# Optimization experiments

Hardware: AMD Instinct MI355X
Metric: run time of the kernel (lower is better)

Reference implementation:

```python
import jax, jax.numpy as jnp
import numpy as np

B, S, D, H = 2, 2048, 1024, 16
HD = D // H  # head_dim = 64


def setup_inputs() -> dict:
    key = jax.random.key(0)
    ks = jax.random.split(key, 6)
    scale = 0.02
    x = jax.random.normal(ks[0], (B, S, D), dtype=jnp.float32)
    Wq = jax.random.normal(ks[1], (D, D), dtype=jnp.float32) * scale
    Wk = jax.random.normal(ks[2], (D, D), dtype=jnp.float32) * scale
    Wv = jax.random.normal(ks[3], (D, D), dtype=jnp.float32) * scale
    Wo = jax.random.normal(ks[4], (D, D), dtype=jnp.float32) * scale
    bo = jnp.zeros((D,), dtype=jnp.float32)
    return {"x": x, "Wq": Wq, "Wk": Wk, "Wv": Wv, "Wo": Wo, "bo": bo}


def reference(x, Wq, Wk, Wv, Wo, bo):
    b, s, _ = x.shape
    # Linear projections (qkv_bias=False), split into heads: [b, h, s, hd]
    def split_heads(t):
        return t.reshape(b, s, H, HD).transpose(0, 2, 1, 3)
    q = split_heads(x @ Wq)
    k = split_heads(x @ Wk)
    v = split_heads(x @ Wv)
    # Scaled dot-product scores: [b, h, s, s]
    scores = jnp.einsum('bhqd,bhkd->bhqk', q, k) / jnp.sqrt(jnp.float32(HD))
    # Causal mask: triu(ones, diagonal=1) positions -> -inf
    causal = jnp.triu(jnp.ones((s, s), dtype=bool), k=1)
    scores = jnp.where(causal, -jnp.inf, scores)
    attn = jax.nn.softmax(scores, axis=-1)
    # dropout p=0.0 (eval-equivalent): identity
    ctx = jnp.einsum('bhqk,bhkd->bhqd', attn, v)  # [b, h, s, hd]
    ctx = ctx.transpose(0, 2, 1, 3).reshape(b, s, D)
    return ctx @ Wo + bo
```

## Files before the change

### kernel.cpp

```cpp
#include <hip/hip_runtime.h>
#include <math.h>

#define BB 2
#define SS 2048
#define DD 1024
#define HH 16
#define HD 64
#define MM (BB * SS)

typedef __bf16 bf16;
typedef __attribute__((ext_vector_type(8))) __bf16 bf16x8;
typedef __attribute__((ext_vector_type(4))) __bf16 bf16x4;
typedef __attribute__((ext_vector_type(4))) float f32x4;

__device__ __forceinline__ void gld_lds16(const void* g, void* l) {
    __builtin_amdgcn_global_load_lds(
        (const __attribute__((address_space(1))) void*)g,
        (__attribute__((address_space(3))) void*)l, 16, 0, 0);
}

__global__ __launch_bounds__(256) void prep(
    const float* __restrict__ x,
    const float* __restrict__ W0, const float* __restrict__ W1,
    const float* __restrict__ W2, const float* __restrict__ W3,
    bf16* __restrict__ xb, bf16* __restrict__ Wt)
{
    __shared__ float tile[32][33];
    const int z = blockIdx.z;
    if (z < 4) {
        const float* W = (z == 0) ? W0 : (z == 1) ? W1 : (z == 2) ? W2 : W3;
        bf16* O = Wt + (size_t)z * DD * DD;
        const int tx = threadIdx.x & 31, ty = threadIdx.x >> 5;
        const int k0 = blockIdx.y * 32, n0 = blockIdx.x * 32;
#pragma unroll
        for (int i = 0; i < 4; ++i)
            tile[ty + i * 8][tx] = W[(size_t)(k0 + ty + i * 8) * DD + n0 + tx];
        __syncthreads();
#pragma unroll
        for (int i = 0; i < 4; ++i)
            O[(size_t)(n0 + ty + i * 8) * DD + k0 + tx] = (bf16)tile[tx][ty + i * 8];
    } else {
        const int lb = (z - 4) * 1024 + blockIdx.y * 32 + blockIdx.x;
        const size_t i = ((size_t)lb * 256 + threadIdx.x) * 8;
        const float4 a = *(const float4*)(x + i);
        const float4 b = *(const float4*)(x + i + 4);
        bf16x8 o;
        o[0] = (bf16)a.x; o[1] = (bf16)a.y; o[2] = (bf16)a.z; o[3] = (bf16)a.w;
        o[4] = (bf16)b.x; o[5] = (bf16)b.y; o[6] = (bf16)b.z; o[7] = (bf16)b.w;
        *(bf16x8*)(xb + i) = o;
    }
}

template<bool SWAP>
__device__ __forceinline__ void mfma_core(
    const bf16* __restrict__ A, const bf16* __restrict__ Bt,
    int bm, int bn, int K, bf16* As, bf16* Bs, f32x4 (&acc)[4][4])
{
    const int t = threadIdx.x;
    const int w = t >> 6;
    const int l16 = t & 15, quad = (t >> 4) & 3;
    const int wr = w >> 1, wc = w & 1;
    const int r0 = t >> 3;
    const int cs = t & 7;

    for (int k0 = 0; k0 < K; k0 += 64) {
#pragma unroll
        for (int j = 0; j < 4; ++j) {
            const int row = j * 32 + r0;
            const int c = (cs - row) & 7;
            gld_lds16(A  + (size_t)(bm + row) * K + k0 + c * 8,
                      As + (j * 32 + w * 8) * 64);
            gld_lds16(Bt + (size_t)(bn + row) * K + k0 + c * 8,
                      Bs + (j * 32 + w * 8) * 64);
        }
        __syncthreads();

#pragma unroll
        for (int h = 0; h < 2; ++h) {
            bf16x8 af[4], bv[4];
#pragma unroll
            for (int i = 0; i < 4; ++i) {
                const int ra = wr * 64 + i * 16 + l16;
                af[i] = *(const bf16x8*)(As + ra * 64 + (((h * 4 + quad) + ra) & 7) * 8);
                const int rb = wc * 64 + i * 16 + l16;
                bv[i] = *(const bf16x8*)(Bs + rb * 64 + (((h * 4 + quad) + rb) & 7) * 8);
            }
#pragma unroll
            for (int mi = 0; mi < 4; ++mi)
#pragma unroll
                for (int ni = 0; ni < 4; ++ni)
                    acc[mi][ni] = SWAP
                        ? __builtin_amdgcn_mfma_f32_16x16x32_bf16(bv[mi], af[ni], acc[mi][ni], 0, 0, 0)
                        : __builtin_amdgcn_mfma_f32_16x16x32_bf16(af[mi], bv[ni], acc[mi][ni], 0, 0, 0);
        }
        __syncthreads();
    }
}

__global__ __launch_bounds__(256) void gemm_qkv(
    const bf16* __restrict__ xb, const bf16* __restrict__ Wt,
    bf16* __restrict__ Qb, bf16* __restrict__ Kb, bf16* __restrict__ Vb)
{
    __shared__ __align__(16) bf16 As[128 * 64];
    __shared__ __align__(16) bf16 Bs[128 * 64];
    const int bm = blockIdx.y * 128, bn = blockIdx.x * 128, z = blockIdx.z;
    const bf16* Wz = Wt + (size_t)z * DD * DD;

    const int t = threadIdx.x;
    const int w = t >> 6, l16 = t & 15, quad = (t >> 4) & 3;
    const int wr = w >> 1, wc = w & 1;

    f32x4 acc[4][4] = {};
    if (z < 2) {
        mfma_core<true>(xb, Wz, bm, bn, DD, As, Bs, acc);
        bf16* outp = (z == 0) ? Qb : Kb;
#pragma unroll
        for (int mi = 0; mi < 4; ++mi) {
            const int feat = bn + wc * 64 + mi * 16 + quad * 4;
            const int h = feat >> 6, hd = feat & 63;
#pragma unroll
            for (int ni = 0; ni < 4; ++ni) {
                const int tok = bm + wr * 64 + ni * 16 + l16;
                const int b = tok >> 11, s = tok & (SS - 1);
                bf16x4 o;
#pragma unroll
                for (int r = 0; r < 4; ++r) o[r] = (bf16)acc[mi][ni][r];
                *(bf16x4*)(outp + ((size_t)((b * HH + h) * SS + s)) * HD + hd) = o;
            }
        }
    } else {
        mfma_core<false>(xb, Wz, bm, bn, DD, As, Bs, acc);
#pragma unroll
        for (int mi = 0; mi < 4; ++mi) {
            const int tok0 = bm + wr * 64 + mi * 16 + quad * 4;
            const int b = tok0 >> 11, s0 = tok0 & (SS - 1);
#pragma unroll
            for (int ni = 0; ni < 4; ++ni) {
                const int feat = bn + wc * 64 + ni * 16 + l16;
                const int h = feat >> 6, hd = feat & 63;
                bf16x4 o;
#pragma unroll
                for (int r = 0; r < 4; ++r) o[r] = (bf16)acc[mi][ni][r];
                *(bf16x4*)(Vb + ((size_t)((b * HH + h) * HD + hd)) * SS + s0) = o;
            }
        }
    }
}

__global__ __launch_bounds__(256) void gemm_out(
    const bf16* __restrict__ ctx, const bf16* __restrict__ Wto,
    const float* __restrict__ bias, float* __restrict__ out)
{
    __shared__ __align__(16) bf16 As[128 * 64];
    __shared__ __align__(16) bf16 Bs[128 * 64];
    const int bm = blockIdx.y * 128, bn = blockIdx.x * 128;

    f32x4 acc[4][4] = {};
    mfma_core<true>(ctx, Wto, bm, bn, DD, As, Bs, acc);

    const int t = threadIdx.x;
    const int w = t >> 6, l16 = t & 15, quad = (t >> 4) & 3;
    const int wr = w >> 1, wc = w & 1;

#pragma unroll
    for (int mi = 0; mi < 4; ++mi) {
        const int feat = bn + wc * 64 + mi * 16 + quad * 4;
        const float4 bb = *(const float4*)(bias + feat);
#pragma unroll
        for (int ni = 0; ni < 4; ++ni) {
            const int tok = bm + wr * 64 + ni * 16 + l16;
            float4 o;
            o.x = acc[mi][ni][0] + bb.x;
            o.y = acc[mi][ni][1] + bb.y;
            o.z = acc[mi][ni][2] + bb.z;
            o.w = acc[mi][ni][3] + bb.w;
            *(float4*)(out + (size_t)tok * DD + feat) = o;
        }
    }
}

#define PROWS 72
__global__ __launch_bounds__(256) void attn_part(
    const bf16* __restrict__ Q, const bf16* __restrict__ K,
    const bf16* __restrict__ Vt, bf16* __restrict__ Op, float* __restrict__ Lp)
{
    __shared__ __align__(16) bf16 Ks[2][64 * 64];
    __shared__ __align__(16) bf16 Vs[2][64 * 64];
    __shared__ __align__(16) bf16 Pl[4][16 * PROWS];

    const int t = threadIdx.x;
    const int w = t >> 6;
    const int lane = t & 63;
    const int l16 = lane & 15, quad = lane >> 4;

    const int L    = blockIdx.x;
    const int bh   = L & 31;
    const int rest = L >> 5;
    const int part = rest & 1;
    const int qg   = 31 - (rest >> 1);
    const int n    = qg + 1;
    const int half = (n + 1) >> 1;
    const int kt_lo = part ? half : 0;
    const int kt_hi = part ? n : half;
    const int q0w  = qg * 64 + w * 16;

    const bf16* Qp = Q  + ((size_t)bh * SS + q0w) * HD;
    const bf16* Kp = K  + (size_t)bh * SS * HD;
    const bf16* Vp = Vt + (size_t)bh * HD * SS;
    bf16* Pw = &Pl[w][0];

    const bf16x8 bQ0 = *(const bf16x8*)(Qp + l16 * HD + quad * 8);
    const bf16x8 bQ1 = *(const bf16x8*)(Qp + l16 * HD + 32 + quad * 8);

    f32x4 accO[4] = {{0,0,0,0},{0,0,0,0},{0,0,0,0},{0,0,0,0}};
    float Lr = 0.f;
    const float cl2 = 0.125f * 1.44269504f;
    const int qrow = q0w + l16;

    const int r8 = lane >> 3, cs = lane & 7;

    if (kt_lo < kt_hi) {
        const int kb0 = kt_lo * 64;
#pragma unroll
        for (int j = 0; j < 2; ++j) {
            const int region = w * 2 + j;
            const int row = region * 8 + r8;
            const int c = (cs - row) & 7;
            gld_lds16(Kp + (size_t)(kb0 + row) * HD + c * 8, &Ks[0][region * 512]);
            gld_lds16(Vp + (size_t)row * SS + kb0 + c * 8, &Vs[0][region * 512]);
        }

        for (int kt = kt_lo; kt < kt_hi; ++kt) {
            const int kb = kt * 64;
            const int buf = (kt - kt_lo) & 1;
            __syncthreads();

            if (kt + 1 < kt_hi) {
                const int kb2 = kb + 64;
#pragma unroll
                for (int j = 0; j < 2; ++j) {
                    const int region = w * 2 + j;
                    const int row = region * 8 + r8;
                    const int c = (cs - row) & 7;
                    gld_lds16(Kp + (size_t)(kb2 + row) * HD + c * 8, &Ks[buf ^ 1][region * 512]);
                    gld_lds16(Vp + (size_t)row * SS + kb2 + c * 8, &Vs[buf ^ 1][region * 512]);
                }
            }

            const bf16* Kbuf = &Ks[buf][0];
            const bf16* Vbuf = &Vs[buf][0];

            f32x4 St[4] = {{0,0,0,0},{0,0,0,0},{0,0,0,0},{0,0,0,0}};
#pragma unroll
            for (int mi = 0; mi < 4; ++mi) {
                const int row = mi * 16 + l16;
                const bf16x8 a0 = *(const bf16x8*)(Kbuf + row * 64 + ((quad + row) & 7) * 8);
                const bf16x8 a1 = *(const bf16x8*)(Kbuf + row * 64 + ((quad + 4 + row) & 7) * 8);
                St[mi] = __builtin_amdgcn_mfma_f32_16x16x32_bf16(a0, bQ0, St[mi], 0, 0, 0);
                St[mi] = __builtin_amdgcn_mfma_f32_16x16x32_bf16(a1, bQ1, St[mi], 0, 0, 0);
            }

            if (kb + 63 > q0w) {
#pragma unroll
                for (int mi = 0; mi < 4; ++mi)
#pragma unroll
                    for (int r = 0; r < 4; ++r)
                        if (kb + mi * 16 + quad * 4 + r > qrow) St[mi][r] = -1e30f;
            }

            float rs = 0.f;
#pragma unroll
            for (int mi = 0; mi < 4; ++mi) {
                bf16x4 pk;
#pragma unroll
                for (int r = 0; r < 4; ++r) {
                    const float p = exp2f(St[mi][r] * cl2);
                    rs += p;
                    pk[r] = (bf16)p;
                }
                *(bf16x4*)(Pw + l16 * PROWS + mi * 16 + quad * 4) = pk;
            }
            rs += __shfl_xor(rs, 16);
            rs += __shfl_xor(rs, 32);
            Lr += rs;

#pragma unroll
            for (int kc = 0; kc < 2; ++kc) {
                const bf16x8 bP = *(const bf16x8*)(Pw + l16 * PROWS + kc * 32 + quad * 8);
#pragma unroll
                for (int mi = 0; mi < 4; ++mi) {
                    const int row = mi * 16 + l16;
                    const bf16x8 aV = *(const bf16x8*)(
                        Vbuf + row * 64 + (((kc * 4 + quad) + row) & 7) * 8);
                    accO[mi] = __builtin_amdgcn_mfma_f32_16x16x32_bf16(aV, bP, accO[mi], 0, 0, 0);
                }
            }
        }
    }

    bf16* op = Op + ((size_t)(part * 32 + bh) * SS + q0w + l16) * HD;
#pragma unroll
    for (int mi = 0; mi < 4; ++mi) {
        bf16x4 o;
#pragma unroll
        for (int r = 0; r < 4; ++r) o[r] = (bf16)accO[mi][r];
        *(bf16x4*)(op + mi * 16 + quad * 4) = o;
    }
    if (quad == 0)
        Lp[(size_t)(part * 32 + bh) * SS + q0w + l16] = Lr;
}

__global__ __launch_bounds__(256) void attn_combine(
    const bf16* __restrict__ Op, const float* __restrict__ Lp,
    bf16* __restrict__ ctx)
{
    const size_t i = ((size_t)blockIdx.x * 256 + threadIdx.x) * 8;
    const int d  = (int)(i & 63);
    const int q  = (int)((i >> 6) & (SS - 1));
    const int bh = (int)(i >> 17);

    const bf16x8 a = *(const bf16x8*)(Op + i);
    const bf16x8 b = *(const bf16x8*)(Op + (size_t)32 * SS * HD + i);
    const size_t lidx = i >> 6;
    const float rinv = 1.0f / (Lp[lidx] + Lp[(size_t)32 * SS + lidx]);

    bf16x8 o;
#pragma unroll
    for (int j = 0; j < 8; ++j)
        o[j] = (bf16)(((float)a[j] + (float)b[j]) * rinv);

    *(bf16x8*)(ctx + ((size_t)((bh >> 4) * SS + q)) * DD + (bh & 15) * 64 + d) = o;
}

extern "C" void kernel_launch(void* const* d_in, const int* in_sizes, int n_in,
                              void* d_out, int out_size, void* d_ws, size_t ws_size,
                              hipStream_t stream)
{
    const float* x  = (const float*)d_in[0];
    const float* Wq = (const float*)d_in[1];
    const float* Wk = (const float*)d_in[2];
    const float* Wv = (const float*)d_in[3];
    const float* Wo = (const float*)d_in[4];
    const float* bo = (const float*)d_in[5];
    float* out = (float*)d_out;

    const size_t chunk = (size_t)MM * DD;
    bf16* xb  = (bf16*)d_ws;
    bf16* Wt  = xb + chunk;
    bf16* Qb  = Wt + 4 * (size_t)DD * DD;
    bf16* Kb  = Qb + chunk;
    bf16* Vb  = Kb + chunk;
    bf16* ctx = Vb + chunk;
    bf16* Op  = ctx + chunk;
    float* Lp = (float*)(Op + 2 * (size_t)32 * SS * HD);

    prep<<<dim3(32, 32, 6), dim3(256), 0, stream>>>(x, Wq, Wk, Wv, Wo, xb, Wt);

    gemm_qkv<<<dim3(DD / 128, MM / 128, 3), dim3(256), 0, stream>>>(xb, Wt, Qb, Kb, Vb);

    attn_part<<<dim3(2048), dim3(256), 0, stream>>>(Qb, Kb, Vb, Op, Lp);
    attn_combine<<<dim3(2048), dim3(256), 0, stream>>>(Op, Lp, ctx);

    gemm_out<<<dim3(DD / 128, MM / 128), dim3(256), 0, stream>>>(
        ctx, Wt + 3 * (size_t)DD * DD, bo, out);
}
```

Baseline: 198.2 us.

## Replace split-K attention and combine with single-pass 128-row attention; retile output GEMM

Attention now gives each block 128 query rows (32 per wave) and walks the full causal key range in one pass. This removes the two-part key split, the partial-output buffers and the separate combine kernel, and normalises directly into ctx. Each K/V tile is reused across twice as many queries, at the cost of fewer blocks (512) and longer, more imbalanced per-block work. The output GEMM switches to 128x64 tiles over a 512-block 1D grid with its own inline load loop. That loop is single-buffered, so it has two syncs per k-step and no prefetch overlap.

```diff
diff --git a/kernel.cpp b/kernel.cpp
--- a/kernel.cpp
+++ b/kernel.cpp
@@ -152,184 +152,221 @@
     const float* __restrict__ bias, float* __restrict__ out)
 {
     __shared__ __align__(16) bf16 As[128 * 64];
-    __shared__ __align__(16) bf16 Bs[128 * 64];
-    const int bm = blockIdx.y * 128, bn = blockIdx.x * 128;
-
-    f32x4 acc[4][4] = {};
-    mfma_core<true>(ctx, Wto, bm, bn, DD, As, Bs, acc);
+    __shared__ __align__(16) bf16 Bs[64 * 64];
+
+    const int L = blockIdx.x;
+    const int bm = (L >> 4) * 128;
+    const int bn = (L & 15) * 64;
 
     const int t = threadIdx.x;
     const int w = t >> 6, l16 = t & 15, quad = (t >> 4) & 3;
     const int wr = w >> 1, wc = w & 1;
-
-#pragma unroll
-    for (int mi = 0; mi < 4; ++mi) {
-        const int feat = bn + wc * 64 + mi * 16 + quad * 4;
+    const int r0 = t >> 3, cs = t & 7;
+
+    f32x4 acc[2][4] = {};
+
+    for (int k0 = 0; k0 < DD; k0 += 64) {
+#pragma unroll
+        for (int j = 0; j < 4; ++j) {
+            const int row = j * 32 + r0;
+            const int c = (cs - row) & 7;
+            gld_lds16(ctx + (size_t)(bm + row) * DD + k0 + c * 8,
+                      As + (j * 32 + w * 8) * 64);
+        }
+#pragma unroll
+        for (int j = 0; j < 2; ++j) {
+            const int row = j * 32 + r0;
+            const int c = (cs - row) & 7;
+            gld_lds16(Wto + (size_t)(bn + row) * DD + k0 + c * 8,
+                      Bs + (j * 32 + w * 8) * 64);
+        }
+        __syncthreads();
+
+#pragma unroll
+        for (int h = 0; h < 2; ++h) {
+            bf16x8 af[4], bv[2];
+#pragma unroll
+            for (int i = 0; i < 4; ++i) {
+                const int ra = wr * 64 + i * 16 + l16;
+                af[i] = *(const bf16x8*)(As + ra * 64 + (((h * 4 + quad) + ra) & 7) * 8);
+            }
+#pragma unroll
+            for (int i = 0; i < 2; ++i) {
+                const int rb = wc * 32 + i * 16 + l16;
+                bv[i] = *(const bf16x8*)(Bs + rb * 64 + (((h * 4 + quad) + rb) & 7) * 8);
+            }
+#pragma unroll
+            for (int fi = 0; fi < 2; ++fi)
+#pragma unroll
+                for (int ti = 0; ti < 4; ++ti)
+                    acc[fi][ti] = __builtin_amdgcn_mfma_f32_16x16x32_bf16(
+                        bv[fi], af[ti], acc[fi][ti], 0, 0, 0);
+        }
+        __syncthreads();
+    }
+
+#pragma unroll
+    for (int fi = 0; fi < 2; ++fi) {
+        const int feat = bn + wc * 32 + fi * 16 + quad * 4;
         const float4 bb = *(const float4*)(bias + feat);
 #pragma unroll
-        for (int ni = 0; ni < 4; ++ni) {
-            const int tok = bm + wr * 64 + ni * 16 + l16;
+        for (int ti = 0; ti < 4; ++ti) {
+            const int tok = bm + wr * 64 + ti * 16 + l16;
             float4 o;
-            o.x = acc[mi][ni][0] + bb.x;
-            o.y = acc[mi][ni][1] + bb.y;
-            o.z = acc[mi][ni][2] + bb.z;
-            o.w = acc[mi][ni][3] + bb.w;
+            o.x = acc[fi][ti][0] + bb.x;
+            o.y = acc[fi][ti][1] + bb.y;
+            o.z = acc[fi][ti][2] + bb.z;
+            o.w = acc[fi][ti][3] + bb.w;
             *(float4*)(out + (size_t)tok * DD + feat) = o;
         }
     }
 }
 
 #define PROWS 72
-__global__ __launch_bounds__(256) void attn_part(
+__global__ __launch_bounds__(256) void attn_flash(
     const bf16* __restrict__ Q, const bf16* __restrict__ K,
-    const bf16* __restrict__ Vt, bf16* __restrict__ Op, float* __restrict__ Lp)
+    const bf16* __restrict__ Vt, bf16* __restrict__ ctx)
 {
     __shared__ __align__(16) bf16 Ks[2][64 * 64];
     __shared__ __align__(16) bf16 Vs[2][64 * 64];
-    __shared__ __align__(16) bf16 Pl[4][16 * PROWS];
+    __shared__ __align__(16) bf16 Pl[4][32 * PROWS];
 
     const int t = threadIdx.x;
     const int w = t >> 6;
     const int lane = t & 63;
     const int l16 = lane & 15, quad = lane >> 4;
 
-    const int L    = blockIdx.x;
-    const int bh   = L & 31;
-    const int rest = L >> 5;
-    const int part = rest & 1;
-    const int qg   = 31 - (rest >> 1);
-    const int n    = qg + 1;
-    const int half = (n + 1) >> 1;
-    const int kt_lo = part ? half : 0;
-    const int kt_hi = part ? n : half;
-    const int q0w  = qg * 64 + w * 16;
+    const int L  = blockIdx.x;
+    const int bh = L & 31;
+    const int qg = 15 - (L >> 5);
+    const int q0w = qg * 128 + w * 32;
 
     const bf16* Qp = Q  + ((size_t)bh * SS + q0w) * HD;
     const bf16* Kp = K  + (size_t)bh * SS * HD;
     const bf16* Vp = Vt + (size_t)bh * HD * SS;
     bf16* Pw = &Pl[w][0];
 
-    const bf16x8 bQ0 = *(const bf16x8*)(Qp + l16 * HD + quad * 8);
-    const bf16x8 bQ1 = *(const bf16x8*)(Qp + l16 * HD + 32 + quad * 8);
-
-    f32x4 accO[4] = {{0,0,0,0},{0,0,0,0},{0,0,0,0},{0,0,0,0}};
-    float Lr = 0.f;
+    bf16x8 bQ[2][2];
+#pragma unroll
+    for (int qs = 0; qs < 2; ++qs)
+#pragma unroll
+        for (int c = 0; c < 2; ++c)
+            bQ[qs][c] = *(const bf16x8*)(Qp + (qs * 16 + l16) * HD + c * 32 + quad * 8);
+
+    f32x4 accO[4][2] = {};
+    float Lr[2] = {0.f, 0.f};
     const float cl2 = 0.125f * 1.44269504f;
-    const int qrow = q0w + l16;
 
     const int r8 = lane >> 3, cs = lane & 7;
-
-    if (kt_lo < kt_hi) {
-        const int kb0 = kt_lo * 64;
-#pragma unroll
-        for (int j = 0; j < 2; ++j) {
-            const int region = w * 2 + j;
-            const int row = region * 8 + r8;
-            const int c = (cs - row) & 7;
-            gld_lds16(Kp + (size_t)(kb0 + row) * HD + c * 8, &Ks[0][region * 512]);
-            gld_lds16(Vp + (size_t)row * SS + kb0 + c * 8, &Vs[0][region * 512]);
-        }
-
-        for (int kt = kt_lo; kt < kt_hi; ++kt) {
-            const int kb = kt * 64;
-            const int buf = (kt - kt_lo) & 1;
-            __syncthreads();
-
-            if (kt + 1 < kt_hi) {
-                const int kb2 = kb + 64;
-#pragma unroll
-                for (int j = 0; j < 2; ++j) {
-                    const int region = w * 2 + j;
-                    const int row = region * 8 + r8;
-                    const int c = (cs - row) & 7;
-                    gld_lds16(Kp + (size_t)(kb2 + row) * HD + c * 8, &Ks[buf ^ 1][region * 512]);
-                    gld_lds16(Vp + (size_t)row * SS + kb2 + c * 8, &Vs[buf ^ 1][region * 512]);
-                }
-            }
-
+    const int nkt = 2 * qg + 2;
+
+#pragma unroll
+    for (int j = 0; j < 2; ++j) {
+        const int region = w * 2 + j;
+        const int row = region * 8 + r8;
+        const int c = (cs - row) & 7;
+        gld_lds16(Kp + (size_t)row * HD + c * 8, &Ks[0][region * 512]);
+        gld_lds16(Vp + (size_t)row * SS + c * 8, &Vs[0][region * 512]);
+    }
+
+    for (int kt = 0; kt < nkt; ++kt) {
+        const int kb = kt * 64;
+        const int buf = kt & 1;
+        __syncthreads();
+
+        if (kt + 1 < nkt) {
+            const int kb2 = kb + 64;
+#pragma unroll
+            for (int j = 0; j < 2; ++j) {
+                const int region = w * 2 + j;
+                const int row = region * 8 + r8;
+                const int c = (cs - row) & 7;
+                gld_lds16(Kp + (size_t)(kb2 + row) * HD + c * 8, &Ks[buf ^ 1][region * 512]);
+                gld_lds16(Vp + (size_t)row * SS + kb2 + c * 8, &Vs[buf ^ 1][region * 512]);
+            }
+        }
+
+        if (kb <= q0w + 31) {
             const bf16* Kbuf = &Ks[buf][0];
             const bf16* Vbuf = &Vs[buf][0];
 
-            f32x4 St[4] = {{0,0,0,0},{0,0,0,0},{0,0,0,0},{0,0,0,0}};
+            f32x4 St[4][2] = {};
 #pragma unroll
             for (int mi = 0; mi < 4; ++mi) {
                 const int row = mi * 16 + l16;
                 const bf16x8 a0 = *(const bf16x8*)(Kbuf + row * 64 + ((quad + row) & 7) * 8);
                 const bf16x8 a1 = *(const bf16x8*)(Kbuf + row * 64 + ((quad + 4 + row) & 7) * 8);
-                St[mi] = __builtin_amdgcn_mfma_f32_16x16x32_bf16(a0, bQ0, St[mi], 0, 0, 0);
-                St[mi] = __builtin_amdgcn_mfma_f32_16x16x32_bf16(a1, bQ1, St[mi], 0, 0, 0);
+#pragma unroll
+                for (int qs = 0; qs < 2; ++qs) {
+                    St[mi][qs] = __builtin_amdgcn_mfma_f32_16x16x32_bf16(a0, bQ[qs][0], St[mi][qs], 0, 0, 0);
+                    St[mi][qs] = __builtin_amdgcn_mfma_f32_16x16x32_bf16(a1, bQ[qs][1], St[mi][qs], 0, 0, 0);
+                }
             }
 
             if (kb + 63 > q0w) {
 #pragma unroll
-                for (int mi = 0; mi < 4; ++mi)
-#pragma unroll
-                    for (int r = 0; r < 4; ++r)
-                        if (kb + mi * 16 + quad * 4 + r > qrow) St[mi][r] = -1e30f;
-            }
-
-            float rs = 0.f;
-#pragma unroll
-            for (int mi = 0; mi < 4; ++mi) {
-                bf16x4 pk;
-#pragma unroll
-                for (int r = 0; r < 4; ++r) {
-                    const float p = exp2f(St[mi][r] * cl2);
-                    rs += p;
-                    pk[r] = (bf16)p;
+                for (int qs = 0; qs < 2; ++qs) {
+                    const int qrow = q0w + qs * 16 + l16;
+#pragma unroll
+                    for (int mi = 0; mi < 4; ++mi)
+#pragma unroll
+                        for (int r = 0; r < 4; ++r)
+                            if (kb + mi * 16 + quad * 4 + r > qrow) St[mi][qs][r] = -1e30f;
                 }
-                *(bf16x4*)(Pw + l16 * PROWS + mi * 16 + quad * 4) = pk;
-            }
-            rs += __shfl_xor(rs, 16);
-            rs += __shfl_xor(rs, 32);
-            Lr += rs;
+            }
+
+#pragma unroll
+            for (int qs = 0; qs < 2; ++qs) {
+                float rs = 0.f;
+#pragma unroll
+                for (int mi = 0; mi < 4; ++mi) {
+                    bf16x4 pk;
+#pragma unroll
+                    for (int r = 0; r < 4; ++r) {
+                        const float p = exp2f(St[mi][qs][r] * cl2);
+                        rs += p;
+                        pk[r] = (bf16)p;
+                    }
+                    *(bf16x4*)(Pw + (qs * 16 + l16) * PROWS + mi * 16 + quad * 4) = pk;
+                }
+                rs += __shfl_xor(rs, 16);
+                rs += __shfl_xor(rs, 32);
+                Lr[qs] += rs;
+            }
 
 #pragma unroll
             for (int kc = 0; kc < 2; ++kc) {
-                const bf16x8 bP = *(const bf16x8*)(Pw + l16 * PROWS + kc * 32 + quad * 8);
+                bf16x8 bP[2];
+#pragma unroll
+                for (int qs = 0; qs < 2; ++qs)
+                    bP[qs] = *(const bf16x8*)(Pw + (qs * 16 + l16) * PROWS + kc * 32 + quad * 8);
 #pragma unroll
                 for (int mi = 0; mi < 4; ++mi) {
                     const int row = mi * 16 + l16;
                     const bf16x8 aV = *(const bf16x8*)(
                         Vbuf + row * 64 + (((kc * 4 + quad) + row) & 7) * 8);
-                    accO[mi] = __builtin_amdgcn_mfma_f32_16x16x32_bf16(aV, bP, accO[mi], 0, 0, 0);
+#pragma unroll
+                    for (int qs = 0; qs < 2; ++qs)
+                        accO[mi][qs] = __builtin_amdgcn_mfma_f32_16x16x32_bf16(
+                            aV, bP[qs], accO[mi][qs], 0, 0, 0);
                 }
             }
         }
     }
 
-    bf16* op = Op + ((size_t)(part * 32 + bh) * SS + q0w + l16) * HD;
-#pragma unroll
-    for (int mi = 0; mi < 4; ++mi) {
-        bf16x4 o;
-#pragma unroll
-        for (int r = 0; r < 4; ++r) o[r] = (bf16)accO[mi][r];
-        *(bf16x4*)(op + mi * 16 + quad * 4) = o;
-    }
-    if (quad == 0)
-        Lp[(size_t)(part * 32 + bh) * SS + q0w + l16] = Lr;
-}
-
-__global__ __launch_bounds__(256) void attn_combine(
-    const bf16* __restrict__ Op, const float* __restrict__ Lp,
-    bf16* __restrict__ ctx)
-{
-    const size_t i = ((size_t)blockIdx.x * 256 + threadIdx.x) * 8;
-    const int d  = (int)(i & 63);
-    const int q  = (int)((i >> 6) & (SS - 1));
-    const int bh = (int)(i >> 17);
-
-    const bf16x8 a = *(const bf16x8*)(Op + i);
-    const bf16x8 b = *(const bf16x8*)(Op + (size_t)32 * SS * HD + i);
-    const size_t lidx = i >> 6;
-    const float rinv = 1.0f / (Lp[lidx] + Lp[(size_t)32 * SS + lidx]);
-
-    bf16x8 o;
-#pragma unroll
-    for (int j = 0; j < 8; ++j)
-        o[j] = (bf16)(((float)a[j] + (float)b[j]) * rinv);
-
-    *(bf16x8*)(ctx + ((size_t)((bh >> 4) * SS + q)) * DD + (bh & 15) * 64 + d) = o;
+    const int b = bh >> 4, h = bh & (HH - 1);
+#pragma unroll
+    for (int qs = 0; qs < 2; ++qs) {
+        const float rinv = 1.0f / Lr[qs];
+        bf16* op = ctx + ((size_t)(b * SS + q0w + qs * 16 + l16)) * DD + h * HD;
+#pragma unroll
+        for (int mi = 0; mi < 4; ++mi) {
+            bf16x4 o;
+#pragma unroll
+            for (int r = 0; r < 4; ++r) o[r] = (bf16)(accO[mi][qs][r] * rinv);
+            *(bf16x4*)(op + mi * 16 + quad * 4) = o;
+        }
+    }
 }
 
 extern "C" void kernel_launch(void* const* d_in, const int* in_sizes, int n_in,
@@ -351,16 +388,13 @@
     bf16* Kb  = Qb + chunk;
     bf16* Vb  = Kb + chunk;
     bf16* ctx = Vb + chunk;
-    bf16* Op  = ctx + chunk;
-    float* Lp = (float*)(Op + 2 * (size_t)32 * SS * HD);
 
     prep<<<dim3(32, 32, 6), dim3(256), 0, stream>>>(x, Wq, Wk, Wv, Wo, xb, Wt);
 
     gemm_qkv<<<dim3(DD / 128, MM / 128, 3), dim3(256), 0, stream>>>(xb, Wt, Qb, Kb, Vb);
 
-    attn_part<<<dim3(2048), dim3(256), 0, stream>>>(Qb, Kb, Vb, Op, Lp);
-    attn_combine<<<dim3(2048), dim3(256), 0, stream>>>(Op, Lp, ctx);
-
-    gemm_out<<<dim3(DD / 128, MM / 128), dim3(256), 0, stream>>>(
+    attn_flash<<<dim3(512), dim3(256), 0, stream>>>(Qb, Kb, Vb, ctx);
+
+    gemm_out<<<dim3(512), dim3(256), 0, stream>>>(
         ctx, Wt + 3 * (size_t)DD * DD, bo, out);
 }
```

New measurement: 206.1 us. 4.0% more time.
